# Performance work log

Measured on AMD Instinct MI355X. Metric: run time of the kernel, lower is better.

The kernel has to match this reference:

```python
import jax, jax.numpy as jnp
import numpy as np

# norse.LIFCell default parameters
DT = 1e-3
TAU_SYN_INV = 200.0   # 1 / 5e-3
TAU_MEM_INV = 100.0   # 1 / 1e-2
V_TH = 1.0
V_LEAK = 0.0
V_RESET = 0.0
ALPHA = 100.0         # SuperSpike surrogate slope

T, B, N_IN, N_HIDDEN, N_OUT = 16, 4096, 784, 256, 10


@jax.custom_vjp
def heaviside(x):
    return (x > 0).astype(x.dtype)

def _h_fwd(x):
    return heaviside(x), x

def _h_bwd(x, g):
    # SuperSpike surrogate: d/dx H(x) ~ 1 / (alpha*|x| + 1)^2
    return (g / (ALPHA * jnp.abs(x) + 1.0) ** 2,)

heaviside.defvjp(_h_fwd, _h_bwd)


def lif_step(inp, v, i):
    """One norse lif_step: Euler-integrate v and i, spike, hard reset."""
    v_decayed = v + DT * TAU_MEM_INV * ((V_LEAK - v) + i)
    i_decayed = i - DT * TAU_SYN_INV * i
    z = heaviside(v_decayed - V_TH)
    v_new = (1.0 - z) * v_decayed + z * V_RESET
    i_new = i_decayed + inp
    return z, v_new, i_new


def setup_inputs() -> dict:
    key = jax.random.key(0)
    k1, k2, k3, k4, k5 = jax.random.split(key, 5)
    # binary spike trains (T, B, N_IN)
    spike_input = (jax.random.uniform(k1, (T, B, N_IN)) < 0.3).astype(jnp.float32)
    lim1 = float(1.0 / np.sqrt(N_IN))
    lim2 = float(1.0 / np.sqrt(N_HIDDEN))
    W1 = jax.random.uniform(k2, (N_HIDDEN, N_IN), minval=-lim1, maxval=lim1, dtype=jnp.float32)
    b1 = jax.random.uniform(k3, (N_HIDDEN,), minval=-lim1, maxval=lim1, dtype=jnp.float32)
    W2 = jax.random.uniform(k4, (N_OUT, N_HIDDEN), minval=-lim2, maxval=lim2, dtype=jnp.float32)
    b2 = jax.random.uniform(k5, (N_OUT,), minval=-lim2, maxval=lim2, dtype=jnp.float32)
    return {"spike_input": spike_input, "W1": W1, "b1": b1, "W2": W2, "b2": b2}


def reference(spike_input, W1, b1, W2, b2):
    batch = spike_input.shape[1]
    nh, no = W1.shape[0], W2.shape[0]
    dtype = spike_input.dtype
    # LIFCell with state=None starts at v=v_leak, i=0
    init = (jnp.full((batch, nh), V_LEAK, dtype), jnp.zeros((batch, nh), dtype),
            jnp.full((batch, no), V_LEAK, dtype), jnp.zeros((batch, no), dtype))

    def step(carry, x_t):
        v1, i1, v2, i2 = carry
        c1 = x_t @ W1.T + b1                 # (B, N_HIDDEN)
        z1, v1, i1 = lif_step(c1, v1, i1)
        c2 = z1 @ W2.T + b2                  # (B, N_OUT)
        z2, v2, i2 = lif_step(c2, v2, i2)
        return (v1, i1, v2, i2), z2

    _, zs = jax.lax.scan(step, init, spike_input)  # zs: (T, B, N_OUT)
    return zs.sum(axis=0)                          # (B, N_OUT)
```

## Files before the change

### kernel.cpp

```cpp
#include <hip/hip_runtime.h>


#define T_STEPS 16
#define B_SZ    4096
#define N_IN    784
#define N_HID   256
#define N_OUT   10
#define M_TOT   (T_STEPS * B_SZ)
#define KPAD    800
#define NT      25

typedef __bf16 bf16x8 __attribute__((ext_vector_type(8)));
typedef float  f32x4  __attribute__((ext_vector_type(4)));
typedef unsigned short ushort_t;
typedef unsigned int   u32;

__device__ __forceinline__ unsigned short bf16_rne(float f) {
    u32 u = __builtin_bit_cast(u32, f);
    u += 0x7fffu + ((u >> 16) & 1u);
    return (unsigned short)(u >> 16);
}

__global__ __launch_bounds__(256) void conv_w(
    const float* __restrict__ W1,
    ushort_t* __restrict__ Whi, ushort_t* __restrict__ Wlo)
{
    const int idx = blockIdx.x * 256 + threadIdx.x;
    if (idx >= N_HID * KPAD) return;
    const int n = idx / KPAD, k = idx % KPAD;
    unsigned short hh = 0, ll = 0;
    if (k < N_IN) {
        const float wv = W1[n * N_IN + k];
        hh = bf16_rne(wv);
        const float hf = __builtin_bit_cast(float, (u32)hh << 16);
        ll = bf16_rne(wv - hf);
    }
    Whi[idx] = hh;
    Wlo[idx] = ll;
}

__device__ __forceinline__ u32 pack_hi16(u32 a, u32 b) {
    return (a >> 16) | (b & 0xffff0000u);
}

__global__ __launch_bounds__(256, 2) void gemm1_mfma(
    const float* __restrict__ X,
    const ushort_t* __restrict__ Whi,
    const ushort_t* __restrict__ Wlo,
    const float* __restrict__ b1,
    float* __restrict__ C)
{
    __shared__ float    Afs[2][128 * 32];
    __shared__ ushort_t Bhs[2][128 * 32];
    __shared__ ushort_t Bls[2][128 * 32];

    const int tid  = threadIdx.x;
    const int lane = tid & 63;
    const int w    = tid >> 6;
    const int wm   = w >> 1;
    const int wn   = w & 1;
    const int bid = blockIdx.x;
    const int lb  = (bid & 7) * 128 + (bid >> 3);
    const int m0  = (lb >> 1) * 128;
    const int n0  = (lb & 1) * 128;
    const int ls  = lane >> 4;
    const int lr  = lane & 15;

    f32x4 acc[4][4];
    #pragma unroll
    for (int i = 0; i < 4; ++i)
        #pragma unroll
        for (int j = 0; j < 4; ++j)
            #pragma unroll
            for (int q = 0; q < 4; ++q)
                acc[i][j][q] = 0.0f;

    auto stage = [&](int bi, int k0, bool clamp) {
        #pragma unroll
        for (int q = 0; q < 4; ++q) {
            const int unit = q * 256 + tid;
            const int row  = unit >> 3;
            const int u4   = ((unit & 7) ^ (row & 7)) << 2;
            const int kk   = (clamp && (k0 + u4 >= N_IN)) ? 0 : (k0 + u4);
            const float* src = X + (size_t)(m0 + row) * N_IN + kk;
            float* dst = &Afs[bi][(q * 256 + (w << 6)) * 4];
            __builtin_amdgcn_global_load_lds(
                (const __attribute__((address_space(1))) void*)src,
                (__attribute__((address_space(3))) void*)dst, 16, 0, 0);
        }
        #pragma unroll
        for (int q = 0; q < 2; ++q) {
            const int unit = q * 256 + tid;
            const int row  = unit >> 2;
            const int u8   = ((unit & 3) ^ (row & 3)) << 3;
            const size_t so = (size_t)(n0 + row) * KPAD + k0 + u8;
            ushort_t* dh = &Bhs[bi][(q * 256 + (w << 6)) * 8];
            ushort_t* dl = &Bls[bi][(q * 256 + (w << 6)) * 8];
            __builtin_amdgcn_global_load_lds(
                (const __attribute__((address_space(1))) void*)(Whi + so),
                (__attribute__((address_space(3))) void*)dh, 16, 0, 0);
            __builtin_amdgcn_global_load_lds(
                (const __attribute__((address_space(1))) void*)(Wlo + so),
                (__attribute__((address_space(3))) void*)dl, 16, 0, 0);
        }
    };

    int aOff0[4], aOff1[4], bOff[4];
    #pragma unroll
    for (int i = 0; i < 4; ++i) {
        const int R = wm * 64 + i * 16 + lr;
        aOff0[i] = R * 32 + ((((2 * ls)     ^ (R & 7))) << 2);
        aOff1[i] = R * 32 + ((((2 * ls + 1) ^ (R & 7))) << 2);
    }
    #pragma unroll
    for (int j = 0; j < 4; ++j) {
        const int R = wn * 64 + j * 16 + lr;
        bOff[j] = R * 32 + ((ls ^ (R & 3)) << 3);
    }

    stage(0, 0, false);

    int buf = 0;
    for (int kt = 0; kt < NT; ++kt) {
        __syncthreads();

        if (kt + 1 < NT)
            stage(buf ^ 1, (kt + 1) * 32, kt + 1 == NT - 1);

        bf16x8 af[4];
        #pragma unroll
        for (int i = 0; i < 4; ++i) {
            const float4 fa = *reinterpret_cast<const float4*>(&Afs[buf][aOff0[i]]);
            const float4 fb = *reinterpret_cast<const float4*>(&Afs[buf][aOff1[i]]);
            uint4 pk;
            pk.x = pack_hi16(__builtin_bit_cast(u32, fa.x), __builtin_bit_cast(u32, fa.y));
            pk.y = pack_hi16(__builtin_bit_cast(u32, fa.z), __builtin_bit_cast(u32, fa.w));
            pk.z = pack_hi16(__builtin_bit_cast(u32, fb.x), __builtin_bit_cast(u32, fb.y));
            pk.w = pack_hi16(__builtin_bit_cast(u32, fb.z), __builtin_bit_cast(u32, fb.w));
            af[i] = __builtin_bit_cast(bf16x8, pk);
        }
        bf16x8 bh[4], bl[4];
        #pragma unroll
        for (int j = 0; j < 4; ++j) {
            bh[j] = *reinterpret_cast<const bf16x8*>(&Bhs[buf][bOff[j]]);
            bl[j] = *reinterpret_cast<const bf16x8*>(&Bls[buf][bOff[j]]);
        }

        #pragma unroll
        for (int i = 0; i < 4; ++i)
            #pragma unroll
            for (int j = 0; j < 4; ++j)
                acc[i][j] = __builtin_amdgcn_mfma_f32_16x16x32_bf16(
                    af[i], bh[j], acc[i][j], 0, 0, 0);
        #pragma unroll
        for (int i = 0; i < 4; ++i)
            #pragma unroll
            for (int j = 0; j < 4; ++j)
                acc[i][j] = __builtin_amdgcn_mfma_f32_16x16x32_bf16(
                    af[i], bl[j], acc[i][j], 0, 0, 0);

        buf ^= 1;
    }

    #pragma unroll
    for (int j = 0; j < 4; ++j) {
        const int col  = n0 + wn * 64 + j * 16 + lr;
        const float bb = b1[col];
        #pragma unroll
        for (int i = 0; i < 4; ++i) {
            const int rbase = m0 + wm * 64 + i * 16 + (ls << 2);
            #pragma unroll
            for (int q = 0; q < 4; ++q)
                C[(size_t)(rbase + q) * N_HID + col] = acc[i][j][q] + bb;
        }
    }
}

__global__ __launch_bounds__(256) void lif1_kernel(float* __restrict__ C1)
{
    const int g = blockIdx.x * 256 + threadIdx.x;
    const size_t stride = (size_t)B_SZ * N_HID;
    float v = 0.0f, cur = 0.0f;
    #pragma unroll
    for (int t = 0; t < T_STEPS; ++t) {
        const size_t off = (size_t)t * stride + g;
        const float c = C1[off];
        const float vd = v + 0.1f * ((0.0f - v) + cur);
        const float id = cur - 0.2f * cur;
        const bool  sp = vd > 1.0f;
        C1[off] = sp ? 1.0f : 0.0f;
        v = sp ? 0.0f : vd;
        cur = id + c;
    }
}

__global__ __launch_bounds__(640) void gemm2_f32(
    const float* __restrict__ Z, const float* __restrict__ W2,
    const float* __restrict__ b2, float* __restrict__ C2)
{
    __shared__ float zs[64 * 268];
    __shared__ float ws[N_OUT * N_HID];
    const int tid = threadIdx.x;
    const int m0 = blockIdx.x * 64;

    for (int idx = tid; idx < 4096; idx += 640) {
        const int r = idx >> 6;
        const int c = (idx & 63) << 2;
        *(float4*)&zs[r * 268 + c] =
            *(const float4*)&Z[(size_t)(m0 + r) * N_HID + c];
    }
    *(float4*)&ws[tid * 4] = *(const float4*)&W2[tid * 4];
    __syncthreads();

    const int o = tid >> 6;
    const int r = tid & 63;
    float acc = b2[o];
    #pragma unroll
    for (int k = 0; k < N_HID; k += 4) {
        const float4 z4 = *(const float4*)&zs[r * 268 + k];
        const float4 w4 = *(const float4*)&ws[o * N_HID + k];
        acc += z4.x * w4.x + z4.y * w4.y + z4.z * w4.z + z4.w * w4.w;
    }
    C2[(size_t)(m0 + r) * N_OUT + o] = acc;
}

__global__ __launch_bounds__(256) void lif2_kernel(
    const float* __restrict__ C2, float* __restrict__ out)
{
    const int g = blockIdx.x * 256 + threadIdx.x;
    const int stride = B_SZ * N_OUT;
    float v = 0.0f, cur = 0.0f, s = 0.0f;
    #pragma unroll
    for (int t = 0; t < T_STEPS; ++t) {
        const float c = C2[t * stride + g];
        const float vd = v + 0.1f * ((0.0f - v) + cur);
        const float id = cur - 0.2f * cur;
        const bool  sp = vd > 1.0f;
        s += sp ? 1.0f : 0.0f;
        v = sp ? 0.0f : vd;
        cur = id + c;
    }
    out[g] = s;
}

extern "C" void kernel_launch(void* const* d_in, const int* in_sizes, int n_in,
                              void* d_out, int out_size, void* d_ws, size_t ws_size,
                              hipStream_t stream)
{
    const float* X  = (const float*)d_in[0];
    const float* W1 = (const float*)d_in[1];
    const float* b1 = (const float*)d_in[2];
    const float* W2 = (const float*)d_in[3];
    const float* b2 = (const float*)d_in[4];
    float* out = (float*)d_out;

    ushort_t* Whi = (ushort_t*)d_ws;
    ushort_t* Wlo = Whi + N_HID * KPAD;
    float* C1 = (float*)((char*)d_ws + (1 << 20));
    float* C2 = C1 + (size_t)M_TOT * N_HID;

    conv_w<<<(N_HID * KPAD + 255) / 256, 256, 0, stream>>>(W1, Whi, Wlo);

    gemm1_mfma<<<M_TOT / 128 * (N_HID / 128), 256, 0, stream>>>(X, Whi, Wlo, b1, C1);

    lif1_kernel<<<(B_SZ * N_HID) / 256, 256, 0, stream>>>(C1);

    gemm2_f32<<<M_TOT / 64, 640, 0, stream>>>(C1, W2, b2, C2);

    lif2_kernel<<<(B_SZ * N_OUT) / 256, 256, 0, stream>>>(C2, out);
}
```

Baseline: 155.9 us.

## Widen gemm1 tile to full N with 512 threads and deeper prefetch

Each block of the first GEMM now covers all 256 hidden columns with 8 waves, so every block reads its 128-row strip of the fp32 spike input only once instead of twice. Loads for step k+2 are issued right after the LDS reads of the current buffer, using explicit vmcnt/lgkmcnt waits and raw s_barrier instead of __syncthreads. MFMA issue priority is raised with s_setprio. The B swizzle is changed for the larger tile. The cost is more LDS per block, which may lower occupancy, and the hand-written waitcnt values are fragile.

```diff
diff --git a/kernel.cpp b/kernel.cpp
--- a/kernel.cpp
+++ b/kernel.cpp
@@ -14,6 +14,11 @@
 typedef float  f32x4  __attribute__((ext_vector_type(4)));
 typedef unsigned short ushort_t;
 typedef unsigned int   u32;
+
+#define GLOAD_LDS(SRC, DST) \
+    __builtin_amdgcn_global_load_lds( \
+        (const __attribute__((address_space(1))) void*)(SRC), \
+        (__attribute__((address_space(3))) void*)(DST), 16, 0, 0)
 
 __device__ __forceinline__ unsigned short bf16_rne(float f) {
     u32 u = __builtin_bit_cast(u32, f);
@@ -43,7 +48,7 @@
     return (a >> 16) | (b & 0xffff0000u);
 }
 
-__global__ __launch_bounds__(256, 2) void gemm1_mfma(
+__global__ __launch_bounds__(512, 2) void gemm1_mfma(
     const float* __restrict__ X,
     const ushort_t* __restrict__ Whi,
     const ushort_t* __restrict__ Wlo,
@@ -51,20 +56,17 @@
     float* __restrict__ C)
 {
     __shared__ float    Afs[2][128 * 32];
-    __shared__ ushort_t Bhs[2][128 * 32];
-    __shared__ ushort_t Bls[2][128 * 32];
+    __shared__ ushort_t Bhs[2][256 * 32];
+    __shared__ ushort_t Bls[2][256 * 32];
 
     const int tid  = threadIdx.x;
     const int lane = tid & 63;
     const int w    = tid >> 6;
-    const int wm   = w >> 1;
-    const int wn   = w & 1;
-    const int bid = blockIdx.x;
-    const int lb  = (bid & 7) * 128 + (bid >> 3);
-    const int m0  = (lb >> 1) * 128;
-    const int n0  = (lb & 1) * 128;
-    const int ls  = lane >> 4;
-    const int lr  = lane & 15;
+    const int wm   = w >> 2;
+    const int wn   = w & 3;
+    const int m0   = blockIdx.x * 128;
+    const int ls   = lane >> 4;
+    const int lr   = lane & 15;
 
     f32x4 acc[4][4];
     #pragma unroll
@@ -75,33 +77,23 @@
             for (int q = 0; q < 4; ++q)
                 acc[i][j][q] = 0.0f;
 
-    auto stage = [&](int bi, int k0, bool clamp) {
-        #pragma unroll
-        for (int q = 0; q < 4; ++q) {
-            const int unit = q * 256 + tid;
-            const int row  = unit >> 3;
-            const int u4   = ((unit & 7) ^ (row & 7)) << 2;
-            const int kk   = (clamp && (k0 + u4 >= N_IN)) ? 0 : (k0 + u4);
-            const float* src = X + (size_t)(m0 + row) * N_IN + kk;
-            float* dst = &Afs[bi][(q * 256 + (w << 6)) * 4];
-            __builtin_amdgcn_global_load_lds(
-                (const __attribute__((address_space(1))) void*)src,
-                (__attribute__((address_space(3))) void*)dst, 16, 0, 0);
-        }
+    auto stage = [&](int bi, int k0) {
         #pragma unroll
         for (int q = 0; q < 2; ++q) {
-            const int unit = q * 256 + tid;
-            const int row  = unit >> 2;
-            const int u8   = ((unit & 3) ^ (row & 3)) << 3;
-            const size_t so = (size_t)(n0 + row) * KPAD + k0 + u8;
-            ushort_t* dh = &Bhs[bi][(q * 256 + (w << 6)) * 8];
-            ushort_t* dl = &Bls[bi][(q * 256 + (w << 6)) * 8];
-            __builtin_amdgcn_global_load_lds(
-                (const __attribute__((address_space(1))) void*)(Whi + so),
-                (__attribute__((address_space(3))) void*)dh, 16, 0, 0);
-            __builtin_amdgcn_global_load_lds(
-                (const __attribute__((address_space(1))) void*)(Wlo + so),
-                (__attribute__((address_space(3))) void*)dl, 16, 0, 0);
+            const int u   = q * 512 + tid;
+            const int row = u >> 3;
+            const int ks  = ((u & 7) ^ (row & 7)) << 2;
+            const int kk  = (k0 + ks < N_IN) ? (k0 + ks) : 0;
+            GLOAD_LDS(X + (size_t)(m0 + row) * N_IN + kk, &Afs[bi][u * 4]);
+        }
+        #pragma unroll
+        for (int q = 0; q < 2; ++q) {
+            const int u   = q * 512 + tid;
+            const int row = u >> 2;
+            const int sl  = ((u & 3) ^ ((row >> 1) & 3)) << 3;
+            const size_t so = (size_t)row * KPAD + k0 + sl;
+            GLOAD_LDS(Whi + so, &Bhs[bi][u * 8]);
+            GLOAD_LDS(Wlo + so, &Bls[bi][u * 8]);
         }
     };
 
@@ -115,19 +107,21 @@
     #pragma unroll
     for (int j = 0; j < 4; ++j) {
         const int R = wn * 64 + j * 16 + lr;
-        bOff[j] = R * 32 + ((ls ^ (R & 3)) << 3);
-    }
-
-    stage(0, 0, false);
-
-    int buf = 0;
+        bOff[j] = R * 32 + ((ls ^ ((R >> 1) & 3)) << 3);
+    }
+
+    stage(0, 0);
+    stage(1, 32);
+
     for (int kt = 0; kt < NT; ++kt) {
-        __syncthreads();
-
-        if (kt + 1 < NT)
-            stage(buf ^ 1, (kt + 1) * 32, kt + 1 == NT - 1);
-
-        bf16x8 af[4];
+        const int buf = kt & 1;
+
+        asm volatile("s_waitcnt vmcnt(6)" ::: "memory");
+        __builtin_amdgcn_sched_barrier(0);
+        __builtin_amdgcn_s_barrier();
+        __builtin_amdgcn_sched_barrier(0);
+
+        bf16x8 af[4], bh[4], bl[4];
         #pragma unroll
         for (int i = 0; i < 4; ++i) {
             const float4 fa = *reinterpret_cast<const float4*>(&Afs[buf][aOff0[i]]);
@@ -139,13 +133,20 @@
             pk.w = pack_hi16(__builtin_bit_cast(u32, fb.z), __builtin_bit_cast(u32, fb.w));
             af[i] = __builtin_bit_cast(bf16x8, pk);
         }
-        bf16x8 bh[4], bl[4];
         #pragma unroll
         for (int j = 0; j < 4; ++j) {
             bh[j] = *reinterpret_cast<const bf16x8*>(&Bhs[buf][bOff[j]]);
             bl[j] = *reinterpret_cast<const bf16x8*>(&Bls[buf][bOff[j]]);
         }
 
+        asm volatile("s_waitcnt lgkmcnt(0)" ::: "memory");
+        __builtin_amdgcn_sched_barrier(0);
+        __builtin_amdgcn_s_barrier();
+        __builtin_amdgcn_sched_barrier(0);
+
+        stage(buf, (kt + 2 < NT) ? (kt + 2) * 32 : 0);
+
+        __builtin_amdgcn_s_setprio(1);
         #pragma unroll
         for (int i = 0; i < 4; ++i)
             #pragma unroll
@@ -158,13 +159,12 @@
             for (int j = 0; j < 4; ++j)
                 acc[i][j] = __builtin_amdgcn_mfma_f32_16x16x32_bf16(
                     af[i], bl[j], acc[i][j], 0, 0, 0);
-
-        buf ^= 1;
+        __builtin_amdgcn_s_setprio(0);
     }
 
     #pragma unroll
     for (int j = 0; j < 4; ++j) {
-        const int col  = n0 + wn * 64 + j * 16 + lr;
+        const int col  = wn * 64 + j * 16 + lr;
         const float bb = b1[col];
         #pragma unroll
         for (int i = 0; i < 4; ++i) {
@@ -261,7 +261,7 @@
 
     conv_w<<<(N_HID * KPAD + 255) / 256, 256, 0, stream>>>(W1, Whi, Wlo);
 
-    gemm1_mfma<<<M_TOT / 128 * (N_HID / 128), 256, 0, stream>>>(X, Whi, Wlo, b1, C1);
+    gemm1_mfma<<<M_TOT / 128, 512, 0, stream>>>(X, Whi, Wlo, b1, C1);
 
     lif1_kernel<<<(B_SZ * N_HID) / 256, 256, 0, stream>>>(C1);
 
```

Measured after the change: 151.4 us. 1.03x faster.
